# Performance work log

Measured on AMD Instinct MI355X. Metric: run time of the kernel, lower is better.

The kernel has to match this reference:

```python
import jax, jax.numpy as jnp
import numpy as np

N_U = 50000
N_I = 50000
E = 800000
E_LBL = 200000
D_IN = 128
HID = 256
OUT = 128


def setup_inputs() -> dict:
    key = jax.random.key(0)
    ks = jax.random.split(key, 32)
    def glorot(k, shp):
        fan = shp[0] + shp[1]
        return jax.random.uniform(k, shp, jnp.float32, -1.0, 1.0) * np.sqrt(6.0 / fan)
    inp = {
        'x_user': jax.random.normal(ks[0], (N_U, D_IN), jnp.float32),
        'x_item': jax.random.normal(ks[1], (N_I, D_IN), jnp.float32),
        'edge_ui': jax.random.randint(ks[2], (2, E), 0, N_U, jnp.int32),
        'edge_iu': jax.random.randint(ks[3], (2, E), 0, N_I, jnp.int32),
        'edge_lbl': jax.random.randint(ks[4], (2, E_LBL), 0, N_U, jnp.int32),
        # layer 0 SAGE params (src_dim=D_IN, dst_dim=D_IN)
        'w_msg_ui0': glorot(ks[5], (D_IN, HID)), 'b_ui0': jnp.zeros((HID,), jnp.float32), 'w_root_ui0': glorot(ks[6], (D_IN, HID)),
        'w_msg_iu0': glorot(ks[7], (D_IN, HID)), 'b_iu0': jnp.zeros((HID,), jnp.float32), 'w_root_iu0': glorot(ks[8], (D_IN, HID)),
        # layer 1 SAGE params (src_dim=HID, dst_dim=HID)
        'w_msg_ui1': glorot(ks[9], (HID, HID)), 'b_ui1': jnp.zeros((HID,), jnp.float32), 'w_root_ui1': glorot(ks[10], (HID, HID)),
        'w_msg_iu1': glorot(ks[11], (HID, HID)), 'b_iu1': jnp.zeros((HID,), jnp.float32), 'w_root_iu1': glorot(ks[12], (HID, HID)),
        # per-node-type output linears on JK concat (2*HID -> OUT)
        'w_lin_u': glorot(ks[13], (2 * HID, OUT)), 'b_lin_u': jnp.zeros((OUT,), jnp.float32),
        'w_lin_i': glorot(ks[14], (2 * HID, OUT)), 'b_lin_i': jnp.zeros((OUT,), jnp.float32),
    }
    return inp


def _sage(x_src, x_dst, edge, w_msg, b_msg, w_root):
    # PyG SAGEConv(aggr='mean'): lin_l(mean_{j in N(i)} x_src[j]) + lin_r(x_dst[i])
    src, dst = edge[0], edge[1]
    n_dst = x_dst.shape[0]
    agg = jax.ops.segment_sum(x_src[src], dst, num_segments=n_dst)          # [n_dst, d_src]
    cnt = jax.ops.segment_sum(jnp.ones((edge.shape[1],), x_src.dtype), dst, num_segments=n_dst)
    mean = agg / jnp.maximum(cnt, 1.0)[:, None]
    return mean @ w_msg + b_msg + x_dst @ w_root


def reference(x_user, x_item, edge_ui, edge_iu, edge_lbl,
              w_msg_ui0, b_ui0, w_root_ui0, w_msg_iu0, b_iu0, w_root_iu0,
              w_msg_ui1, b_ui1, w_root_ui1, w_msg_iu1, b_iu1, w_root_iu1,
              w_lin_u, b_lin_u, w_lin_i, b_lin_i):
    # ----- encode: 2 HeteroConv(SAGEConv) layers -----
    item0 = _sage(x_user, x_item, edge_ui, w_msg_ui0, b_ui0, w_root_ui0)    # user->item
    user0 = _sage(x_item, x_user, edge_iu, b_msg=b_iu0, w_msg=w_msg_iu0, x_src=None, x_dst=None, edge=None, w_root=None) if False else _sage(x_item, x_user, edge_iu, w_msg_iu0, b_iu0, w_root_iu0)  # item->user
    item1 = _sage(user0, item0, edge_ui, w_msg_ui1, b_ui1, w_root_ui1)
    user1 = _sage(item0, user0, edge_iu, w_msg_iu1, b_iu1, w_root_iu1)
    # ----- JumpingKnowledge 'cat' + per-node-type linear -----
    z_user = jnp.concatenate([user0, user1], axis=-1) @ w_lin_u + b_lin_u   # [N_U, OUT]
    z_item = jnp.concatenate([item0, item1], axis=-1) @ w_lin_i + b_lin_i   # [N_I, OUT]
    # ----- decode: dot product over candidate edges (user, buys, item) -----
    pred = jnp.sum(z_user[edge_lbl[0]] * z_item[edge_lbl[1]], axis=-1)      # [E_LBL]
    return pred
```

## Files before the change

### kernel.cpp

```cpp
#include <hip/hip_runtime.h>

#define NU 50000
#define NI 50000
#define NE 800000
#define NLBL 200000
#define DIN 128
#define HID 256
#define DOUT 128

#define NSLICE 64
#define SLICE_SZ 12500
#define HALF_N 25000

typedef unsigned short ushort_t;
typedef __attribute__((ext_vector_type(8))) short bf16x8;
typedef __attribute__((ext_vector_type(4))) float f32x4;

__device__ __forceinline__ float bf2f(unsigned int u_shifted) {
    union { unsigned int i; float f; } v;
    v.i = u_shifted;
    return v.f;
}
__device__ __forceinline__ float bf_lo(unsigned int u) { return bf2f(u << 16); }
__device__ __forceinline__ float bf_hi(unsigned int u) { return bf2f(u & 0xffff0000u); }
__device__ __forceinline__ ushort_t f2bf(float f) {
    union { float f; unsigned int i; } v;
    v.f = f;
    unsigned int r = (v.i + 0x7FFFu + ((v.i >> 16) & 1u)) >> 16;
    return (ushort_t)r;
}
__device__ __forceinline__ void load_lds16(const ushort_t* g, ushort_t* s) {
    __builtin_amdgcn_global_load_lds(
        (const __attribute__((address_space(1))) void*)g,
        (__attribute__((address_space(3))) void*)s, 16, 0, 0);
}

#define CVT_PER 782
#define CVT_B (2 * CVT_PER)
#define SA_B 512

struct CvtArgs {
    const float* xu; ushort_t* xbu; const float* xi; ushort_t* xbi;
};

__global__ __launch_bounds__(256) void cvt_kernel(CvtArgs a) {
    int b = blockIdx.x;
    int t = threadIdx.x;
    int which = (b >= CVT_PER);
    int cb = which ? b - CVT_PER : b;
    const float4* in = (const float4*)(which ? a.xi : a.xu);
    uint2* outp = (uint2*)(which ? a.xbi : a.xbu);
    const int n4 = NU * DIN / 4;
#pragma unroll
    for (int k = 0; k < 8; ++k) {
        int i = cb * 2048 + k * 256 + t;
        if (i < n4) {
            float4 v = in[i];
            uint2 o;
            o.x = (unsigned int)f2bf(v.x) | ((unsigned int)f2bf(v.y) << 16);
            o.y = (unsigned int)f2bf(v.z) | ((unsigned int)f2bf(v.w) << 16);
            outp[i] = o;
        }
    }
}

struct HistSaArgs {
    const int *eui, *eiu;
    ushort_t* cnt_s;
    const float *wm_ui1, *wr_ui1, *wm_iu1, *wr_iu1, *lin_i, *lin_u;
    float *G_i, *S_i, *G_u, *S_u;
    int* scan_part;
};

__global__ __launch_bounds__(256) void hist_sa(HistSaArgs a) {
    __shared__ unsigned int cnt[HALF_N / 2];
    int b = blockIdx.x, t = threadIdx.x;
    if (b < 256) {
        int g = b >> 7, s = (b >> 1) & 63, half = b & 1;
        for (int i = t; i < HALF_N / 2; i += 256) cnt[i] = 0;
        __syncthreads();
        const int* dst = (g ? a.eiu : a.eui) + NE;
        int hbase = half * HALF_N;
        int e0 = s * SLICE_SZ;
        for (int i = e0 + t; i < e0 + SLICE_SZ; i += 256) {
            int d = dst[i] - hbase;
            if ((unsigned)d < (unsigned)HALF_N)
                atomicAdd(&cnt[d >> 1], 1u << ((d & 1) * 16));
        }
        __syncthreads();
        unsigned int* outp = (unsigned int*)(a.cnt_s + ((size_t)(g * NSLICE + s)) * 50000 + hbase);
        for (int i = t; i < HALF_N / 2; i += 256) outp[i] = cnt[i];
    } else if (b < 256 + SA_B) {
        int r2 = b - 256;
        int which = r2 >> 7;
        int e = (r2 & 127) * 256 + t;
        int k = e >> 7, n = e & 127;
        const float* W = (which == 0) ? a.wm_ui1 : (which == 1) ? a.wr_ui1
                       : (which == 2) ? a.wm_iu1 : a.wr_iu1;
        const float* L = (which < 2) ? a.lin_i : a.lin_u;
        float* O = (which == 0) ? a.G_i : (which == 1) ? a.S_i
                 : (which == 2) ? a.G_u : a.S_u;
        float s = (which & 1) ? L[k * 128 + n] : 0.f;
#pragma unroll 4
        for (int j = 0; j < HID; ++j) s += W[k * HID + j] * L[(HID + j) * 128 + n];
        O[k * 128 + n] = s;
    } else {
        if (t < 64) a.scan_part[t] = 0;
    }
}

struct SscanP2Args {
    ushort_t* cnt_s;
    int* totals;
    int* scan_part;
    const float *wm_ui0, *wr_ui0, *wm_iu0, *wr_iu0;
    const float *G_i, *S_i, *G_u, *S_u;
    const float *b_ui0, *b_iu0, *b_ui1, *b_iu1, *lin_i, *lin_u, *bl_i, *bl_u;
    ushort_t *VT1_i, *VT2_i, *VT3_i, *VT1_u, *VT2_u, *VT3_u;
    float *bz_i, *bz_u;
};

__global__ __launch_bounds__(256) void sscan_prep2(SscanP2Args a) {
    __shared__ int wsum[4];
    int b = blockIdx.x, t = threadIdx.x;
    if (b < 392) {
        if (b == 0 && t == 0) a.totals[100000] = 2 * NE;
        int idx = b * 256 + t;
        int run = 0;
        if (idx < 100000) {
            int g = idx / 50000, node = idx - g * 50000;
            size_t base = (size_t)g * NSLICE * 50000 + node;
#pragma unroll 4
            for (int s = 0; s < NSLICE; ++s) {
                size_t o = base + (size_t)s * 50000;
                int c = a.cnt_s[o];
                a.cnt_s[o] = (ushort_t)run;
                run += c;
            }
            a.totals[idx] = run;
        }
        int s = run;
#pragma unroll
        for (int off = 32; off > 0; off >>= 1) s += __shfl_down(s, off, 64);
        if ((t & 63) == 0) wsum[t >> 6] = s;
        __syncthreads();
        if (t == 0) atomicAdd(&a.scan_part[b >> 3], wsum[0] + wsum[1] + wsum[2] + wsum[3]);
    } else {
        int task = b - 392;
        if (task < 384) {
            int v = task >> 6;
            int e = (task & 63) * 256 + t;
            int k = e >> 7, n = e & 127;
            const float *A1, *X1, *A2 = nullptr, *X2 = nullptr;
            ushort_t* O;
            switch (v) {
                case 0: A1 = a.wm_ui0; X1 = a.S_i; A2 = a.wr_iu0; X2 = a.G_i; O = a.VT1_i; break;
                case 1: A1 = a.wr_ui0; X1 = a.S_i; O = a.VT2_i; break;
                case 2: A1 = a.wm_iu0; X1 = a.G_i; O = a.VT3_i; break;
                case 3: A1 = a.wm_iu0; X1 = a.S_u; A2 = a.wr_ui0; X2 = a.G_u; O = a.VT1_u; break;
                case 4: A1 = a.wr_iu0; X1 = a.S_u; O = a.VT2_u; break;
                default: A1 = a.wm_ui0; X1 = a.G_u; O = a.VT3_u; break;
            }
            float s = 0.f;
#pragma unroll 4
            for (int j = 0; j < HID; ++j) s += A1[k * HID + j] * X1[j * 128 + n];
            if (A2) {
#pragma unroll 4
                for (int j = 0; j < HID; ++j) s += A2[k * HID + j] * X2[j * 128 + n];
            }
            O[n * 128 + k] = f2bf(s);
        } else if (t < 128) {
            int user = task - 384;
            int n = t;
            const float* S = user ? a.S_u : a.S_i;
            const float* G = user ? a.G_u : a.G_i;
            const float* b_own0 = user ? a.b_iu0 : a.b_ui0;
            const float* b_oth0 = user ? a.b_ui0 : a.b_iu0;
            const float* b_own1 = user ? a.b_iu1 : a.b_ui1;
            const float* lin = user ? a.lin_u : a.lin_i;
            const float* bl = user ? a.bl_u : a.bl_i;
            float* o = user ? a.bz_u : a.bz_i;
            float s = bl[n];
            for (int j = 0; j < HID; ++j)
                s += b_own0[j] * S[j * 128 + n] + b_oth0[j] * G[j * 128 + n] +
                     b_own1[j] * lin[(HID + j) * 128 + n];
            o[n] = s;
        }
    }
}

__global__ __launch_bounds__(256) void scan3(int* __restrict__ d, const int* __restrict__ part,
                                             int n, int nb) {
    __shared__ int wsum[4];
    __shared__ int blockoff_sh;
    int b = blockIdx.x, t = threadIdx.x;
    int lane = t & 63, wv = t >> 6;
    if (t < 64) {
        int v = (t < nb) ? part[t] : 0;
        int incl = v;
#pragma unroll
        for (int off = 1; off < 64; off <<= 1) {
            int tv = __shfl_up(incl, off, 64);
            if (t >= off) incl += tv;
        }
        if (t == b) blockoff_sh = incl - v;
    }
    int i0 = b * 2048 + t * 8;
    int v[8];
    int tsum = 0;
#pragma unroll
    for (int k = 0; k < 8; ++k) {
        v[k] = (i0 + k < n) ? d[i0 + k] : 0;
        tsum += v[k];
    }
    int incl = tsum;
#pragma unroll
    for (int off = 1; off < 64; off <<= 1) {
        int tv = __shfl_up(incl, off, 64);
        if (lane >= off) incl += tv;
    }
    if (lane == 63) wsum[wv] = incl;
    __syncthreads();
    int woff = 0;
    for (int w = 0; w < wv; ++w) woff += wsum[w];
    int run = blockoff_sh + woff + (incl - tsum);
#pragma unroll
    for (int k = 0; k < 8; ++k) {
        if (i0 + k < n) d[i0 + k] = run;
        run += v[k];
    }
}

__global__ __launch_bounds__(256) void fill_lds(const int* __restrict__ eui,
                                                const int* __restrict__ eiu,
                                                const ushort_t* __restrict__ cnt_s,
                                                const int* __restrict__ rowstart,
                                                ushort_t* __restrict__ csr) {
    __shared__ unsigned int off[HALF_N / 2];
    int b = blockIdx.x, t = threadIdx.x;
    int g = b >> 7, s = (b >> 1) & 63, half = b & 1;
    const unsigned int* st =
        (const unsigned int*)(cnt_s + ((size_t)(g * NSLICE + s)) * 50000 + half * HALF_N);
    for (int i = t; i < HALF_N / 2; i += 256) off[i] = st[i];
    __syncthreads();
    const int* src = g ? eiu : eui;
    const int* dst = src + NE;
    const int* rs = rowstart + g * 50000;
    int hbase = half * HALF_N;
    int e0 = s * SLICE_SZ;
    for (int i = e0 + t; i < e0 + SLICE_SZ; i += 256) {
        int dd = dst[i];
        int d = dd - hbase;
        if ((unsigned)d < (unsigned)HALF_N) {
            unsigned old = atomicAdd(&off[d >> 1], 1u << ((d & 1) * 16));
            int rel = (int)((old >> ((d & 1) * 16)) & 0xffffu);
            csr[(size_t)rs[dd] + rel] = (ushort_t)src[i];
        }
    }
}

struct AggJob { const int* sp; const ushort_t* csr; const ushort_t* x; ushort_t* out; int n; };
struct AggJobs2 { AggJob j[2]; };

__global__ __launch_bounds__(256) void agg_din(AggJobs2 js) {
    AggJob jb = js.j[blockIdx.y];
    const int half = blockIdx.z;
    int wave = (int)((blockIdx.x * 256u + threadIdx.x) >> 6);
    int lane = threadIdx.x & 63;
    const int l = lane & 15;
    const int h = lane >> 4;
    int w4 = wave * 4;
    if (w4 >= jb.n) return;
    int w = w4 + h;
    int s0 = jb.sp[w];
    int s1 = jb.sp[w + 1];
    int cnt = s1 - s0;
    float sc = (cnt > 0) ? 1.0f / (float)cnt : 0.0f;
    int cmax = cnt;
    {
        int c1 = __shfl_xor(cmax, 16, 64); cmax = (cmax > c1) ? cmax : c1;
        int c2 = __shfl_xor(cmax, 32, 64); cmax = (cmax > c2) ? cmax : c2;
    }
    const uint2* xp = (const uint2*)jb.x + half * 16;
    float f0 = 0.f, f1 = 0.f, f2 = 0.f, f3 = 0.f;
#define ACC4(m, u)                                                     \
    f0 = fmaf(m, bf_lo(u.x), f0); f1 = fmaf(m, bf_hi(u.x), f1);        \
    f2 = fmaf(m, bf_lo(u.y), f2); f3 = fmaf(m, bf_hi(u.y), f3);
    for (int chunk = 0; chunk < cmax; chunk += 16) {
        int mh = cnt - chunk;
        int safe = (mh > 0) ? ((l < mh) ? l : mh - 1) : 0;
        int vidx = (int)jb.csr[s0 + chunk + safe];
        int mm = cmax - chunk;
        if (mm > 16) mm = 16;
        int j = 0;
        for (; j + 3 < mm; j += 4) {
            int i0 = __shfl(vidx, j, 16);
            int i1 = __shfl(vidx, j + 1, 16);
            int i2 = __shfl(vidx, j + 2, 16);
            int i3 = __shfl(vidx, j + 3, 16);
            float m0 = (j < mh) ? 1.f : 0.f;
            float m1 = (j + 1 < mh) ? 1.f : 0.f;
            float m2 = (j + 2 < mh) ? 1.f : 0.f;
            float m3 = (j + 3 < mh) ? 1.f : 0.f;
            uint2 u0 = xp[(size_t)((j < mh) ? i0 : 0) * 32 + l];
            uint2 u1 = xp[(size_t)((j + 1 < mh) ? i1 : 0) * 32 + l];
            uint2 u2 = xp[(size_t)((j + 2 < mh) ? i2 : 0) * 32 + l];
            uint2 u3 = xp[(size_t)((j + 3 < mh) ? i3 : 0) * 32 + l];
            ACC4(m0, u0);
            ACC4(m1, u1);
            ACC4(m2, u2);
            ACC4(m3, u3);
        }
        for (; j < mm; ++j) {
            int i0 = __shfl(vidx, j, 16);
            float m0 = (j < mh) ? 1.f : 0.f;
            uint2 u0 = xp[(size_t)((j < mh) ? i0 : 0) * 32 + l];
            ACC4(m0, u0);
        }
    }
#undef ACC4
    uint2 o;
    o.x = (unsigned int)f2bf(f0 * sc) | ((unsigned int)f2bf(f1 * sc) << 16);
    o.y = (unsigned int)f2bf(f2 * sc) | ((unsigned int)f2bf(f3 * sc) << 16);
    ((uint2*)jb.out)[(size_t)w * 32 + half * 16 + l] = o;
}

struct GemmJob {
    const ushort_t* A[3];
    const ushort_t* WT[3];
    int K[3];
    const float* bias;
    void* C;
};
struct GemmJobs2 { GemmJob j[2]; };

template <int NP, typename OutT>
__global__ __launch_bounds__(256) void gemmN(GemmJobs2 js, int M, int N) {
    GemmJob jb = js.j[blockIdx.z];
    __shared__ ushort_t sA[128 * 32];
    __shared__ ushort_t sB[128 * 32];
    const int tid = threadIdx.x;
    const int lane = tid & 63;
    const int wv = tid >> 6;
    const int wm = wv & 1, wn = wv >> 1;
    const int bm = blockIdx.y * 128, bn = blockIdx.x * 128;

    f32x4 acc[4][4] = {};

    const int srow = tid >> 2;
    const int scol = (tid & 3) * 8;

#pragma unroll
    for (int part = 0; part < NP; ++part) {
        const ushort_t* A = jb.A[part];
        const ushort_t* WT = jb.WT[part];
        const int K = jb.K[part];
        int ar0 = bm + srow;       if (ar0 > M - 1) ar0 = M - 1;
        int ar1 = bm + 64 + srow;  if (ar1 > M - 1) ar1 = M - 1;
        const size_t aoff0 = (size_t)ar0 * K + scol;
        const size_t aoff1 = (size_t)ar1 * K + scol;
        const size_t boff0 = (size_t)(bn + srow) * K + scol;
        const size_t boff1 = (size_t)(bn + 64 + srow) * K + scol;
        for (int k0 = 0; k0 < K; k0 += 32) {
            __syncthreads();
            load_lds16(A + aoff0 + k0, sA + tid * 8);
            load_lds16(A + aoff1 + k0, sA + 2048 + tid * 8);
            load_lds16(WT + boff0 + k0, sB + tid * 8);
            load_lds16(WT + boff1 + k0, sB + 2048 + tid * 8);
            __syncthreads();
            const ushort_t* pA = sA + ((wm * 64 + (lane & 15)) * 32 + (lane >> 4) * 8);
            const ushort_t* pB = sB + ((wn * 64 + (lane & 15)) * 32 + (lane >> 4) * 8);
            bf16x8 af[4], bfr[4];
#pragma unroll
            for (int mt = 0; mt < 4; ++mt) af[mt] = *(const bf16x8*)(pA + mt * 512);
#pragma unroll
            for (int nt = 0; nt < 4; ++nt) bfr[nt] = *(const bf16x8*)(pB + nt * 512);
#pragma unroll
            for (int mt = 0; mt < 4; ++mt)
#pragma unroll
                for (int nt = 0; nt < 4; ++nt)
                    acc[mt][nt] = __builtin_amdgcn_mfma_f32_16x16x32_bf16(
                        af[mt], bfr[nt], acc[mt][nt], 0, 0, 0);
        }
    }

#pragma unroll
    for (int mt = 0; mt < 4; ++mt) {
#pragma unroll
        for (int r = 0; r < 4; ++r) {
            int row = bm + wm * 64 + mt * 16 + (lane >> 4) * 4 + r;
            if (row >= M) continue;
#pragma unroll
            for (int nt = 0; nt < 4; ++nt) {
                int col = bn + wn * 64 + nt * 16 + (lane & 15);
                float v = acc[mt][nt][r] + jb.bias[col];
                if constexpr (sizeof(OutT) == 2)
                    ((ushort_t*)jb.C)[(size_t)row * N + col] = f2bf(v);
                else
                    ((float*)jb.C)[(size_t)row * N + col] = v;
            }
        }
    }
}

__global__ void decode_kernel(const int* __restrict__ lbl, const ushort_t* __restrict__ zu,
                              const ushort_t* __restrict__ zi, float* __restrict__ out, int n) {
    int gid = blockIdx.x * blockDim.x + threadIdx.x;
    int wave = gid >> 6;
    int lane = threadIdx.x & 63;
    int q = lane >> 4;
    int l = lane & 15;
    int e = wave * 4 + q;
    if (e >= n) return;
    int u = lbl[e];
    int it = lbl[n + e];
    uint4 a = ((const uint4*)zu)[(size_t)u * 16 + l];
    uint4 b = ((const uint4*)zi)[(size_t)it * 16 + l];
    float s = bf_lo(a.x) * bf_lo(b.x) + bf_hi(a.x) * bf_hi(b.x) +
              bf_lo(a.y) * bf_lo(b.y) + bf_hi(a.y) * bf_hi(b.y) +
              bf_lo(a.z) * bf_lo(b.z) + bf_hi(a.z) * bf_hi(b.z) +
              bf_lo(a.w) * bf_lo(b.w) + bf_hi(a.w) * bf_hi(b.w);
#pragma unroll
    for (int off = 8; off > 0; off >>= 1) s += __shfl_down(s, off, 16);
    if (l == 0) out[e] = s;
}

extern "C" void kernel_launch(void* const* d_in, const int* in_sizes, int n_in,
                              void* d_out, int out_size, void* d_ws, size_t ws_size,
                              hipStream_t stream) {
    const float* x_user = (const float*)d_in[0];
    const float* x_item = (const float*)d_in[1];
    const int* edge_ui = (const int*)d_in[2];
    const int* edge_iu = (const int*)d_in[3];
    const int* edge_lbl = (const int*)d_in[4];
    const float* w_msg_ui0 = (const float*)d_in[5];
    const float* b_ui0 = (const float*)d_in[6];
    const float* w_root_ui0 = (const float*)d_in[7];
    const float* w_msg_iu0 = (const float*)d_in[8];
    const float* b_iu0 = (const float*)d_in[9];
    const float* w_root_iu0 = (const float*)d_in[10];
    const float* w_msg_ui1 = (const float*)d_in[11];
    const float* b_ui1 = (const float*)d_in[12];
    const float* w_root_ui1 = (const float*)d_in[13];
    const float* w_msg_iu1 = (const float*)d_in[14];
    const float* b_iu1 = (const float*)d_in[15];
    const float* w_root_iu1 = (const float*)d_in[16];
    const float* w_lin_u = (const float*)d_in[17];
    const float* b_lin_u = (const float*)d_in[18];
    const float* w_lin_i = (const float*)d_in[19];
    const float* b_lin_i = (const float*)d_in[20];
    float* out = (float*)d_out;

    char* p = (char*)d_ws;
    ushort_t* user0 = (ushort_t*)p;  p += (size_t)NU * HID * 2;
    ushort_t* item0 = (ushort_t*)p;  p += (size_t)NI * HID * 2;
    ushort_t* user1 = (ushort_t*)p;  p += (size_t)NU * HID * 2;
    ushort_t* item1 = (ushort_t*)p;  p += (size_t)NI * HID * 2;
    (void)user0; (void)item0; (void)user1; (void)item1;
    ushort_t* A_i  = (ushort_t*)p;   p += (size_t)NI * DIN * 2;
    ushort_t* A_u  = (ushort_t*)p;   p += (size_t)NU * DIN * 2;
    ushort_t* B_i  = (ushort_t*)p;   p += (size_t)NI * DIN * 2;
    ushort_t* B_u  = (ushort_t*)p;   p += (size_t)NU * DIN * 2;
    ushort_t* xb_u  = (ushort_t*)p;  p += (size_t)NU * DIN * 2;
    ushort_t* xb_i  = (ushort_t*)p;  p += (size_t)NI * DIN * 2;
    ushort_t* z_user = (ushort_t*)p; p += (size_t)NU * DOUT * 2;
    ushort_t* z_item = (ushort_t*)p; p += (size_t)NI * DOUT * 2;
    int* totals     = (int*)p;       p += (size_t)(100000 + 64) * 4;
    ushort_t* csr   = (ushort_t*)p;  p += (size_t)2 * NE * 2;
    ushort_t* cnt_s = (ushort_t*)p;  p += (size_t)2 * NSLICE * 50000 * 2;
    int* scan_part  = (int*)p;       p += 64 * 4;
    float* G_i = (float*)p; p += (size_t)HID * 128 * 4;
    float* S_i = (float*)p; p += (size_t)HID * 128 * 4;
    float* G_u = (float*)p; p += (size_t)HID * 128 * 4;
    float* S_u = (float*)p; p += (size_t)HID * 128 * 4;
    ushort_t* VT1_i = (ushort_t*)p; p += (size_t)128 * 128 * 2;
    ushort_t* VT2_i = (ushort_t*)p; p += (size_t)128 * 128 * 2;
    ushort_t* VT3_i = (ushort_t*)p; p += (size_t)128 * 128 * 2;
    ushort_t* VT1_u = (ushort_t*)p; p += (size_t)128 * 128 * 2;
    ushort_t* VT2_u = (ushort_t*)p; p += (size_t)128 * 128 * 2;
    ushort_t* VT3_u = (ushort_t*)p; p += (size_t)128 * 128 * 2;
    float* bz_i = (float*)p; p += 128 * 4;
    float* bz_u = (float*)p; p += 128 * 4;

    const int NCNT = 100000;
    const int NB = (NCNT + 2047) / 2048;

    CvtArgs cv = { x_user, xb_u, x_item, xb_i };
    cvt_kernel<<<CVT_B, 256, 0, stream>>>(cv);

    HistSaArgs hs;
    hs.eui = edge_ui; hs.eiu = edge_iu; hs.cnt_s = cnt_s;
    hs.wm_ui1 = w_msg_ui1; hs.wr_ui1 = w_root_ui1;
    hs.wm_iu1 = w_msg_iu1; hs.wr_iu1 = w_root_iu1;
    hs.lin_i = w_lin_i; hs.lin_u = w_lin_u;
    hs.G_i = G_i; hs.S_i = S_i; hs.G_u = G_u; hs.S_u = S_u;
    hs.scan_part = scan_part;
    hist_sa<<<256 + SA_B + 1, 256, 0, stream>>>(hs);

    SscanP2Args sp;
    sp.cnt_s = cnt_s; sp.totals = totals; sp.scan_part = scan_part;
    sp.wm_ui0 = w_msg_ui0; sp.wr_ui0 = w_root_ui0;
    sp.wm_iu0 = w_msg_iu0; sp.wr_iu0 = w_root_iu0;
    sp.G_i = G_i; sp.S_i = S_i; sp.G_u = G_u; sp.S_u = S_u;
    sp.b_ui0 = b_ui0; sp.b_iu0 = b_iu0; sp.b_ui1 = b_ui1; sp.b_iu1 = b_iu1;
    sp.lin_i = w_lin_i; sp.lin_u = w_lin_u; sp.bl_i = b_lin_i; sp.bl_u = b_lin_u;
    sp.VT1_i = VT1_i; sp.VT2_i = VT2_i; sp.VT3_i = VT3_i;
    sp.VT1_u = VT1_u; sp.VT2_u = VT2_u; sp.VT3_u = VT3_u;
    sp.bz_i = bz_i; sp.bz_u = bz_u;
    sscan_prep2<<<392 + 386, 256, 0, stream>>>(sp);

    scan3<<<NB, 256, 0, stream>>>(totals, scan_part, NCNT, NB);

    fill_lds<<<256, 256, 0, stream>>>(edge_ui, edge_iu, cnt_s, totals, csr);

    {
        AggJobs2 aj = {{{totals, csr, xb_u, A_i, NI},
                        {totals + 50000, csr, xb_i, A_u, NU}}};
        agg_din<<<dim3(3125, 2, 2), 256, 0, stream>>>(aj);
    }
    {
        AggJobs2 aj = {{{totals, csr, A_u, B_i, NI},
                        {totals + 50000, csr, A_i, B_u, NU}}};
        agg_din<<<dim3(3125, 2, 2), 256, 0, stream>>>(aj);
    }

    {
        GemmJobs2 gj = {{{{A_i, xb_i, B_i}, {VT1_i, VT2_i, VT3_i}, {DIN, DIN, DIN}, bz_i, z_item},
                         {{A_u, xb_u, B_u}, {VT1_u, VT2_u, VT3_u}, {DIN, DIN, DIN}, bz_u, z_user}}};
        gemmN<3, ushort_t><<<dim3(DOUT / 128, (NU + 127) / 128, 2), 256, 0, stream>>>(gj, NU, DOUT);
    }

    decode_kernel<<<(((NLBL + 3) / 4) * 64 + 255) / 256, 256, 0, stream>>>(
        edge_lbl, z_user, z_item, out, NLBL);
}
```

Measured before the change: 372.5 us.

## Fuse bf16 conversion into histogram kernel and double edge slice count

The standalone fp32→bf16 conversion kernel becomes extra blocks of the histogram/weight-precompute kernel, which removes one launch and lets the conversion overlap with the atomic-heavy histogram blocks. The edge histogram and CSR fill now use 128 slices of 6250 edges instead of 64 slices of 12500. That doubles the block count for those two phases to raise parallelism and shorten each block. In exchange, the per-slice count arrays double, so the slice scan and fill must read twice as much per-slice count data. Unused layer-output workspace buffers are also dropped.

```diff
diff --git a/kernel.cpp b/kernel.cpp
--- a/kernel.cpp
+++ b/kernel.cpp
@@ -8,8 +8,8 @@
 #define HID 256
 #define DOUT 128
 
-#define NSLICE 64
-#define SLICE_SZ 12500
+#define NSLICE 128
+#define SLICE_SZ 6250
 #define HALF_N 25000
 
 typedef unsigned short ushort_t;
@@ -38,45 +38,22 @@
 #define CVT_PER 782
 #define CVT_B (2 * CVT_PER)
 #define SA_B 512
-
-struct CvtArgs {
-    const float* xu; ushort_t* xbu; const float* xi; ushort_t* xbi;
-};
-
-__global__ __launch_bounds__(256) void cvt_kernel(CvtArgs a) {
-    int b = blockIdx.x;
-    int t = threadIdx.x;
-    int which = (b >= CVT_PER);
-    int cb = which ? b - CVT_PER : b;
-    const float4* in = (const float4*)(which ? a.xi : a.xu);
-    uint2* outp = (uint2*)(which ? a.xbi : a.xbu);
-    const int n4 = NU * DIN / 4;
-#pragma unroll
-    for (int k = 0; k < 8; ++k) {
-        int i = cb * 2048 + k * 256 + t;
-        if (i < n4) {
-            float4 v = in[i];
-            uint2 o;
-            o.x = (unsigned int)f2bf(v.x) | ((unsigned int)f2bf(v.y) << 16);
-            o.y = (unsigned int)f2bf(v.z) | ((unsigned int)f2bf(v.w) << 16);
-            outp[i] = o;
-        }
-    }
-}
-
-struct HistSaArgs {
+#define HIST_B (2 * NSLICE * 2)
+
+struct P1Args {
     const int *eui, *eiu;
     ushort_t* cnt_s;
     const float *wm_ui1, *wr_ui1, *wm_iu1, *wr_iu1, *lin_i, *lin_u;
     float *G_i, *S_i, *G_u, *S_u;
     int* scan_part;
+    const float* xu; ushort_t* xbu; const float* xi; ushort_t* xbi;
 };
 
-__global__ __launch_bounds__(256) void hist_sa(HistSaArgs a) {
+__global__ __launch_bounds__(256) void phase1(P1Args a) {
     __shared__ unsigned int cnt[HALF_N / 2];
     int b = blockIdx.x, t = threadIdx.x;
-    if (b < 256) {
-        int g = b >> 7, s = (b >> 1) & 63, half = b & 1;
+    if (b < HIST_B) {
+        int g = b >> 8, s = (b >> 1) & 127, half = b & 1;
         for (int i = t; i < HALF_N / 2; i += 256) cnt[i] = 0;
         __syncthreads();
         const int* dst = (g ? a.eiu : a.eui) + NE;
@@ -90,8 +67,8 @@
         __syncthreads();
         unsigned int* outp = (unsigned int*)(a.cnt_s + ((size_t)(g * NSLICE + s)) * 50000 + hbase);
         for (int i = t; i < HALF_N / 2; i += 256) outp[i] = cnt[i];
-    } else if (b < 256 + SA_B) {
-        int r2 = b - 256;
+    } else if (b < HIST_B + SA_B) {
+        int r2 = b - HIST_B;
         int which = r2 >> 7;
         int e = (r2 & 127) * 256 + t;
         int k = e >> 7, n = e & 127;
@@ -104,8 +81,26 @@
 #pragma unroll 4
         for (int j = 0; j < HID; ++j) s += W[k * HID + j] * L[(HID + j) * 128 + n];
         O[k * 128 + n] = s;
+    } else if (b == HIST_B + SA_B) {
+        if (t < 64) a.scan_part[t] = 0;
     } else {
-        if (t < 64) a.scan_part[t] = 0;
+        int cb = b - (HIST_B + SA_B + 1);
+        int which = (cb >= CVT_PER);
+        if (which) cb -= CVT_PER;
+        const float4* in = (const float4*)(which ? a.xi : a.xu);
+        uint2* outp = (uint2*)(which ? a.xbi : a.xbu);
+        const int n4 = NU * DIN / 4;
+#pragma unroll
+        for (int k = 0; k < 8; ++k) {
+            int i = cb * 2048 + k * 256 + t;
+            if (i < n4) {
+                float4 v = in[i];
+                uint2 o;
+                o.x = (unsigned int)f2bf(v.x) | ((unsigned int)f2bf(v.y) << 16);
+                o.y = (unsigned int)f2bf(v.z) | ((unsigned int)f2bf(v.w) << 16);
+                outp[i] = o;
+            }
+        }
     }
 }
 
@@ -238,7 +233,7 @@
                                                 ushort_t* __restrict__ csr) {
     __shared__ unsigned int off[HALF_N / 2];
     int b = blockIdx.x, t = threadIdx.x;
-    int g = b >> 7, s = (b >> 1) & 63, half = b & 1;
+    int g = b >> 8, s = (b >> 1) & 127, half = b & 1;
     const unsigned int* st =
         (const unsigned int*)(cnt_s + ((size_t)(g * NSLICE + s)) * 50000 + half * HALF_N);
     for (int i = t; i < HALF_N / 2; i += 256) off[i] = st[i];
@@ -452,11 +447,6 @@
     float* out = (float*)d_out;
 
     char* p = (char*)d_ws;
-    ushort_t* user0 = (ushort_t*)p;  p += (size_t)NU * HID * 2;
-    ushort_t* item0 = (ushort_t*)p;  p += (size_t)NI * HID * 2;
-    ushort_t* user1 = (ushort_t*)p;  p += (size_t)NU * HID * 2;
-    ushort_t* item1 = (ushort_t*)p;  p += (size_t)NI * HID * 2;
-    (void)user0; (void)item0; (void)user1; (void)item1;
     ushort_t* A_i  = (ushort_t*)p;   p += (size_t)NI * DIN * 2;
     ushort_t* A_u  = (ushort_t*)p;   p += (size_t)NU * DIN * 2;
     ushort_t* B_i  = (ushort_t*)p;   p += (size_t)NI * DIN * 2;
@@ -485,17 +475,15 @@
     const int NCNT = 100000;
     const int NB = (NCNT + 2047) / 2048;
 
-    CvtArgs cv = { x_user, xb_u, x_item, xb_i };
-    cvt_kernel<<<CVT_B, 256, 0, stream>>>(cv);
-
-    HistSaArgs hs;
-    hs.eui = edge_ui; hs.eiu = edge_iu; hs.cnt_s = cnt_s;
-    hs.wm_ui1 = w_msg_ui1; hs.wr_ui1 = w_root_ui1;
-    hs.wm_iu1 = w_msg_iu1; hs.wr_iu1 = w_root_iu1;
-    hs.lin_i = w_lin_i; hs.lin_u = w_lin_u;
-    hs.G_i = G_i; hs.S_i = S_i; hs.G_u = G_u; hs.S_u = S_u;
-    hs.scan_part = scan_part;
-    hist_sa<<<256 + SA_B + 1, 256, 0, stream>>>(hs);
+    P1Args p1;
+    p1.eui = edge_ui; p1.eiu = edge_iu; p1.cnt_s = cnt_s;
+    p1.wm_ui1 = w_msg_ui1; p1.wr_ui1 = w_root_ui1;
+    p1.wm_iu1 = w_msg_iu1; p1.wr_iu1 = w_root_iu1;
+    p1.lin_i = w_lin_i; p1.lin_u = w_lin_u;
+    p1.G_i = G_i; p1.S_i = S_i; p1.G_u = G_u; p1.S_u = S_u;
+    p1.scan_part = scan_part;
+    p1.xu = x_user; p1.xbu = xb_u; p1.xi = x_item; p1.xbi = xb_i;
+    phase1<<<HIST_B + SA_B + 1 + CVT_B, 256, 0, stream>>>(p1);
 
     SscanP2Args sp;
     sp.cnt_s = cnt_s; sp.totals = totals; sp.scan_part = scan_part;
@@ -511,7 +499,7 @@
 
     scan3<<<NB, 256, 0, stream>>>(totals, scan_part, NCNT, NB);
 
-    fill_lds<<<256, 256, 0, stream>>>(edge_ui, edge_iu, cnt_s, totals, csr);
+    fill_lds<<<HIST_B, 256, 0, stream>>>(edge_ui, edge_iu, cnt_s, totals, csr);
 
     {
         AggJobs2 aj = {{{totals, csr, xb_u, A_i, NI},
```

Result: no change. 366.3 us (-1.7%).
